# Kernel optimization log

Hardware: AMD Instinct MI355X
Metric: run time of the kernel (lower is better)

The kernel has to match this reference:

```python
import jax, jax.numpy as jnp
import numpy as np

N_NODES = 100000
IN_DIM = 512
HIDDEN = 64
NUM_CLASSES = 40
N_EDGES = 3200000


def setup_inputs() -> dict:
    key = jax.random.key(0)
    k1, k2, k3, k4, k5 = jax.random.split(key, 5)
    x = jax.random.normal(k1, (N_NODES, IN_DIM), dtype=jnp.float32)
    edge_index = jax.random.randint(k2, (2, N_EDGES), 0, N_NODES, dtype=jnp.int64)
    # Glorot init like PyG GCNConv, zero bias
    s1 = (6.0 / (IN_DIM + HIDDEN)) ** 0.5
    W1 = jax.random.uniform(k3, (IN_DIM, HIDDEN), jnp.float32, -s1, s1)
    b1 = jnp.zeros((HIDDEN,), jnp.float32)
    s2 = (6.0 / (HIDDEN + NUM_CLASSES)) ** 0.5
    W2 = jax.random.uniform(k4, (HIDDEN, NUM_CLASSES), jnp.float32, -s2, s2)
    b2 = jnp.zeros((NUM_CLASSES,), jnp.float32)
    return {"x": x, "edge_index": edge_index, "W1": W1, "b1": b1, "W2": W2, "b2": b2}


def _gcn_norm(edge_index, num_nodes):
    # Add self-loops, compute symmetric normalization D^-1/2 A D^-1/2 (PyG GCNConv default).
    loop = jnp.arange(num_nodes, dtype=edge_index.dtype)
    src = jnp.concatenate([edge_index[0], loop])
    dst = jnp.concatenate([edge_index[1], loop])
    deg = jax.ops.segment_sum(jnp.ones_like(src, dtype=jnp.float32), dst, num_segments=num_nodes)
    dinv = jnp.where(deg > 0, jax.lax.rsqrt(deg), 0.0)
    norm = dinv[src] * dinv[dst]  # [E+N]
    return src, dst, norm


def _gcn_conv(x, src, dst, norm, W, b, num_nodes):
    h = x @ W                                # [N, F_out]
    msg = h[src] * norm[:, None]             # gather + scale, [E+N, F_out]
    out = jax.ops.segment_sum(msg, dst, num_segments=num_nodes)  # scatter-add
    return out + b


def reference(x, edge_index, W1, b1, W2, b2):
    n = x.shape[0]
    src, dst, norm = _gcn_norm(edge_index, n)
    h = _gcn_conv(x, src, dst, norm, W1, b1, n)
    h = jax.nn.relu(h)
    # F.dropout(training=False) is identity in eval mode
    h = _gcn_conv(h, src, dst, norm, W2, b2, n)
    return jax.nn.log_softmax(h, axis=1)
```

## Files before the change

kernel.cpp:

```cpp
#include <hip/hip_runtime.h>
#include <hip/hip_bf16.h>
#include <cmath>

#define NN 100000
#define IND 512
#define HID 64
#define NC  40
#define BWN 256
#define NBKT ((NN + BWN - 1) / BWN)
#define NBIN_BLOCKS 100

typedef unsigned int uint32;
typedef unsigned short ushort;
using short8 = __attribute__((ext_vector_type(8))) short;
using f32x4  = __attribute__((ext_vector_type(4))) float;

__device__ inline float bf_lo(uint32 u) { return __uint_as_float(u << 16); }
__device__ inline float bf_hi(uint32 u) { return __uint_as_float(u & 0xFFFF0000u); }
__device__ inline uint32 f2bf(float f) {
    uint32 u = __float_as_uint(f);
    return (u + 0x7FFFu + ((u >> 16) & 1u)) >> 16;
}
__device__ inline uint32 pack2bf(float a, float b) { return f2bf(a) | (f2bf(b) << 16); }


__global__ __launch_bounds__(256) void zero_kernel(int* __restrict__ ghist, int n) {
    int i = blockIdx.x * blockDim.x + threadIdx.x;
    if (i < n) ghist[i] = 0;
}

__global__ __launch_bounds__(256) void bhist_kernel(const int* __restrict__ dst,
                                                    int* __restrict__ ghist, int E) {
    __shared__ int hist[NBKT];
    int t = threadIdx.x;
    for (int i = t; i < NBKT; i += 256) hist[i] = 0;
    __syncthreads();
    for (int e = blockIdx.x * 256 + t; e < E; e += gridDim.x * 256)
        atomicAdd(&hist[dst[e] >> 8], 1);
    __syncthreads();
    for (int i = t; i < NBKT; i += 256)
        if (hist[i]) atomicAdd(&ghist[i], hist[i]);
}

__global__ __launch_bounds__(512) void bscan_kernel(const int* __restrict__ ghist,
                                                    int* __restrict__ bbase,
                                                    int* __restrict__ gcursor) {
    __shared__ int sh[512];
    int t = threadIdx.x;
    int v = (t < NBKT) ? ghist[t] : 0;
    sh[t] = v;
    __syncthreads();
    for (int off = 1; off < 512; off <<= 1) {
        int u = (t >= off) ? sh[t - off] : 0;
        __syncthreads();
        sh[t] += u;
        __syncthreads();
    }
    int ex = sh[t] - v;
    if (t < NBKT) { bbase[t] = ex; gcursor[t] = ex; }
    if (t == NBKT - 1) bbase[NBKT] = ex + v;
}

__global__ __launch_bounds__(512) void bin_kernel(const int* __restrict__ src,
                                                  const int* __restrict__ dst,
                                                  int* __restrict__ gcursor,
                                                  int* __restrict__ packed, int E) {
    __shared__ int hist[NBKT], base[NBKT], cur[NBKT];
    int b = blockIdx.x, t = threadIdx.x;
    int epb = (E + gridDim.x - 1) / gridDim.x;
    int lo = b * epb;
    int hi = lo + epb; if (hi > E) hi = E;
    for (int i = t; i < NBKT; i += 512) { hist[i] = 0; cur[i] = 0; }
    __syncthreads();
    for (int e = lo + t; e < hi; e += 512) atomicAdd(&hist[dst[e] >> 8], 1);
    __syncthreads();
    for (int i = t; i < NBKT; i += 512)
        if (hist[i]) base[i] = atomicAdd(&gcursor[i], hist[i]);
    __syncthreads();
    for (int e = lo + t; e < hi; e += 512) {
        int d = dst[e], s = src[e];
        int bk = d >> 8;
        int pos = base[bk] + atomicAdd(&cur[bk], 1);
        packed[pos] = ((d & 255) << 17) | s;
    }
}

__global__ __launch_bounds__(256) void csr_bucket_kernel(const int* __restrict__ packed,
                                                         const int* __restrict__ bbase,
                                                         int* __restrict__ rowptr,
                                                         int* __restrict__ colx,
                                                         float* __restrict__ dinv, int E) {
    __shared__ int hist[BWN], pfx[BWN], cur[BWN];
    int b = blockIdx.x, t = threadIdx.x;
    int nlo = b * BWN;
    int ncnt = NN - nlo; if (ncnt > BWN) ncnt = BWN;
    int ebeg = bbase[b], eend = bbase[b + 1];
    hist[t] = 0;
    __syncthreads();
    for (int e = ebeg + t; e < eend; e += 256) atomicAdd(&hist[packed[e] >> 17], 1);
    __syncthreads();
    int h = hist[t];
    pfx[t] = h;
    __syncthreads();
    for (int off = 1; off < 256; off <<= 1) {
        int u = (t >= off) ? pfx[t - off] : 0;
        __syncthreads();
        pfx[t] += u;
        __syncthreads();
    }
    int excl = pfx[t] - h;
    cur[t] = excl;
    int g = nlo + t;
    if (t < ncnt) {
        rowptr[g] = ebeg + excl;
        dinv[g] = rsqrtf((float)(h + 1));
    }
    if (b == 0 && t == 0) rowptr[NN] = E;
    __syncthreads();
    for (int e = ebeg + t; e < eend; e += 256) {
        int p = packed[e];
        int dl = p >> 17;
        int s = p & 0x1FFFF;
        int pos = ebeg + atomicAdd(&cur[dl], 1);
        colx[pos] = s;
    }
}


__global__ __launch_bounds__(256) void wt_kernel(const float* __restrict__ W1,
                                                 const float* __restrict__ W2,
                                                 ushort* __restrict__ w1t,
                                                 ushort* __restrict__ w2t) {
    int id = blockIdx.x * blockDim.x + threadIdx.x;
    if (id < IND * HID) {
        int n = id & 63, k = id >> 6;
        w1t[(size_t)n * IND + k] = (ushort)f2bf(W1[(size_t)k * HID + n]);
    } else if (id < IND * HID + 48 * HID) {
        int id2 = id - IND * HID;
        int n = id2 >> 6, k = id2 & 63;
        w2t[id2] = (n < NC) ? (ushort)f2bf(W2[(size_t)k * NC + n]) : (ushort)0;
    }
}


__global__ __launch_bounds__(256) void gemm1_mfma(const float* __restrict__ x,
                                                  const ushort* __restrict__ w1t,
                                                  const float* __restrict__ dinv,
                                                  ushort* __restrict__ hs, int M) {
    __shared__ ushort As[64 * 64];
    __shared__ ushort Bs[64 * 64];
    char* Ab = (char*)As;
    char* Bb = (char*)Bs;

    int t = threadIdx.x;
    int row0 = blockIdx.x * 64;

    int srow = t >> 2;
    int klane = t & 3;
    int grow = row0 + srow; if (grow > M - 1) grow = M - 1;
    const float* xrow = x + (size_t)grow * IND;
    const char* wrow = (const char*)(w1t + (size_t)srow * IND);
    int swrow = srow * 128;
    int swx = (srow & 7) << 4;

    int l = t & 63;
    int w = t >> 6;
    int lr = l & 15;
    int lk = (l >> 4) * 16;
    int arow_b = (w * 16 + lr) * 128;
    int aswz = ((w * 16 + lr) & 7) << 4;

    f32x4 acc[4] = {};

    float4 rx[4]; uint2 rw[4];
#pragma unroll
    for (int i = 0; i < 4; ++i) {
        rx[i] = *(const float4*)(xrow + i * 16 + klane * 4);
        rw[i] = *(const uint2*)(wrow + i * 32 + klane * 8);
    }

    for (int k0 = 0; k0 < IND; k0 += 64) {
#pragma unroll
        for (int i = 0; i < 4; ++i) {
            int kb = i * 32 + klane * 8;
            uint2 pkd;
            pkd.x = pack2bf(rx[i].x, rx[i].y);
            pkd.y = pack2bf(rx[i].z, rx[i].w);
            *(uint2*)(Ab + swrow + (kb ^ swx)) = pkd;
            *(uint2*)(Bb + swrow + (kb ^ swx)) = rw[i];
        }
        __syncthreads();

        if (k0 + 64 < IND) {
#pragma unroll
            for (int i = 0; i < 4; ++i) {
                rx[i] = *(const float4*)(xrow + k0 + 64 + i * 16 + klane * 4);
                rw[i] = *(const uint2*)(wrow + (k0 + 64) * 2 + i * 32 + klane * 8);
            }
        }

        short8 a0 = *(const short8*)(Ab + arow_b + ((0 + lk) ^ aswz));
        short8 a1 = *(const short8*)(Ab + arow_b + ((64 + lk) ^ aswz));
#pragma unroll
        for (int ns = 0; ns < 4; ++ns) {
            int brow = ns * 16 + lr;
            int bswz = (brow & 7) << 4;
            short8 b0 = *(const short8*)(Bb + brow * 128 + ((0 + lk) ^ bswz));
            short8 b1 = *(const short8*)(Bb + brow * 128 + ((64 + lk) ^ bswz));
            acc[ns] = __builtin_amdgcn_mfma_f32_16x16x32_bf16(a0, b0, acc[ns], 0, 0, 0);
            acc[ns] = __builtin_amdgcn_mfma_f32_16x16x32_bf16(a1, b1, acc[ns], 0, 0, 0);
        }
        __syncthreads();
    }

    int rbase = row0 + w * 16 + (l >> 4) * 4;
    float dv[4];
#pragma unroll
    for (int j = 0; j < 4; ++j) dv[j] = (rbase + j < M) ? dinv[rbase + j] : 0.f;
#pragma unroll
    for (int ns = 0; ns < 4; ++ns) {
        int col = ns * 16 + lr;
#pragma unroll
        for (int j = 0; j < 4; ++j) {
            int row = rbase + j;
            if (row < M) hs[(size_t)row * HID + col] = (ushort)f2bf(acc[ns][j] * dv[j]);
        }
    }
}


__global__ __launch_bounds__(256) void agg1_kernel(const uint32* __restrict__ hs,
                                                   const int* __restrict__ rowptr,
                                                   const int* __restrict__ colx,
                                                   const float* __restrict__ dinv,
                                                   const float* __restrict__ b1,
                                                   uint32* __restrict__ h1) {
    int node = (blockIdx.x * blockDim.x + threadIdx.x) >> 5;
    int l = threadIdx.x & 31;
    if (node >= NN) return;
    int beg = rowptr[node], end = rowptr[node + 1];
    uint32 u = hs[(size_t)node * 32 + l];
    float a0 = bf_lo(u), a1 = bf_hi(u);
    int e = beg;
    int n8 = beg + ((end - beg) & ~7);
    for (; e < n8; e += 8) {
        int c[8];
#pragma unroll
        for (int j = 0; j < 8; ++j) c[j] = __builtin_nontemporal_load(&colx[e + j]);
        uint32 uu[8];
#pragma unroll
        for (int j = 0; j < 8; ++j) uu[j] = hs[(size_t)c[j] * 32 + l];
#pragma unroll
        for (int j = 0; j < 8; ++j) { a0 += bf_lo(uu[j]); a1 += bf_hi(uu[j]); }
    }
    for (; e < end; ++e) {
        uint32 ue = hs[(size_t)__builtin_nontemporal_load(&colx[e]) * 32 + l];
        a0 += bf_lo(ue); a1 += bf_hi(ue);
    }
    float d = dinv[node];
    float2 bb = *(const float2*)(b1 + 2 * l);
    float v0 = a0 * d + bb.x;
    float v1 = a1 * d + bb.y;
    v0 = v0 > 0.f ? v0 : 0.f;
    v1 = v1 > 0.f ? v1 : 0.f;
    __builtin_nontemporal_store(pack2bf(v0, v1), &h1[(size_t)node * 32 + l]);
}


__global__ __launch_bounds__(256) void gemm2_mfma(const ushort* __restrict__ h1,
                                                  const ushort* __restrict__ w2t,
                                                  const float* __restrict__ dinv,
                                                  ushort* __restrict__ h2b, int M) {
    int t = threadIdx.x;
    int w = t >> 6, l = t & 63;
    int lr = l & 15, lh = l >> 4;
    int row0 = blockIdx.x * 64 + w * 16;
    int arow = row0 + lr; if (arow > M - 1) arow = M - 1;
    const ushort* hrow = h1 + (size_t)arow * HID;

    f32x4 acc[3] = {};
#pragma unroll
    for (int ks = 0; ks < 2; ++ks) {
        short8 a = *(const short8*)(hrow + ks * 32 + lh * 8);
#pragma unroll
        for (int ns = 0; ns < 3; ++ns) {
            short8 b = *(const short8*)(w2t + (size_t)(ns * 16 + lr) * HID + ks * 32 + lh * 8);
            acc[ns] = __builtin_amdgcn_mfma_f32_16x16x32_bf16(a, b, acc[ns], 0, 0, 0);
        }
    }

    int rbase = row0 + lh * 4;
    float dv[4];
#pragma unroll
    for (int j = 0; j < 4; ++j) dv[j] = (rbase + j < M) ? dinv[rbase + j] : 0.f;
#pragma unroll
    for (int ns = 0; ns < 3; ++ns) {
        int col = ns * 16 + lr;
        if (col < NC) {
#pragma unroll
            for (int j = 0; j < 4; ++j) {
                int row = rbase + j;
                if (row < M) h2b[(size_t)row * NC + col] = (ushort)f2bf(acc[ns][j] * dv[j]);
            }
        }
    }
}


__global__ __launch_bounds__(256) void agg2_kernel(const uint32* __restrict__ h2b,
                                                   const int* __restrict__ rowptr,
                                                   const int* __restrict__ colx,
                                                   const float* __restrict__ dinv,
                                                   const float* __restrict__ b2,
                                                   float* __restrict__ out) {
    int node = (blockIdx.x * blockDim.x + threadIdx.x) >> 5;
    int l = threadIdx.x & 31;
    if (node >= NN) return;
    bool act = l < 20;
    int beg = rowptr[node], end = rowptr[node + 1];
    float a0 = 0.f, a1 = 0.f;
    if (act) {
        uint32 u = h2b[(size_t)node * 20 + l];
        a0 = bf_lo(u); a1 = bf_hi(u);
    }
    int e = beg;
    int n8 = beg + ((end - beg) & ~7);
    for (; e < n8; e += 8) {
        int c[8];
#pragma unroll
        for (int j = 0; j < 8; ++j) c[j] = __builtin_nontemporal_load(&colx[e + j]);
        if (act) {
            uint32 uu[8];
#pragma unroll
            for (int j = 0; j < 8; ++j) uu[j] = h2b[(size_t)c[j] * 20 + l];
#pragma unroll
            for (int j = 0; j < 8; ++j) { a0 += bf_lo(uu[j]); a1 += bf_hi(uu[j]); }
        }
    }
    for (; e < end; ++e) {
        int c = __builtin_nontemporal_load(&colx[e]);
        if (act) {
            uint32 ue = h2b[(size_t)c * 20 + l];
            a0 += bf_lo(ue); a1 += bf_hi(ue);
        }
    }

    float d = dinv[node];
    float v0 = -INFINITY, v1 = -INFINITY;
    if (act) {
        float2 bb = *(const float2*)(b2 + 2 * l);
        v0 = a0 * d + bb.x;
        v1 = a1 * d + bb.y;
    }
    float m = fmaxf(v0, v1);
#pragma unroll
    for (int off = 16; off; off >>= 1) m = fmaxf(m, __shfl_xor(m, off));
    float s = act ? (expf(v0 - m) + expf(v1 - m)) : 0.f;
#pragma unroll
    for (int off = 16; off; off >>= 1) s += __shfl_xor(s, off);
    if (act) {
        float ls = logf(s);
        __builtin_nontemporal_store(v0 - m - ls, &out[(size_t)node * NC + 2 * l]);
        __builtin_nontemporal_store(v1 - m - ls, &out[(size_t)node * NC + 2 * l + 1]);
    }
}


extern "C" void kernel_launch(void* const* d_in, const int* in_sizes, int n_in,
                              void* d_out, int out_size, void* d_ws, size_t ws_size,
                              hipStream_t stream) {
    const float* x  = (const float*)d_in[0];
    const int* ei   = (const int*)d_in[1];
    const float* W1 = (const float*)d_in[2];
    const float* b1 = (const float*)d_in[3];
    const float* W2 = (const float*)d_in[4];
    const float* b2 = (const float*)d_in[5];
    float* out = (float*)d_out;

    const int E = in_sizes[1] / 2;
    const int* src = ei;
    const int* dst = ei + E;

    char* p = (char*)d_ws;
    size_t off = 0;
    auto carve = [&](size_t bytes) {
        void* q = p + off;
        off = (off + bytes + 255) & ~(size_t)255;
        return q;
    };
    int* ghist    = (int*)carve((size_t)NBKT * 4);
    int* bbase    = (int*)carve((size_t)(NBKT + 1) * 4);
    int* gcursor  = (int*)carve((size_t)NBKT * 4);
    int* rowptr   = (int*)carve((size_t)(NN + 1) * 4);
    float* dinv   = (float*)carve((size_t)NN * 4);
    int* colx     = (int*)carve((size_t)E * 4);
    ushort* w1t   = (ushort*)carve((size_t)IND * HID * 2);
    ushort* w2t   = (ushort*)carve((size_t)48 * HID * 2);
    ushort* hs    = (ushort*)carve((size_t)NN * HID * 2);
    ushort* h2b   = (ushort*)carve((size_t)NN * NC * 2);
    uint32* h1    = (uint32*)carve((size_t)NN * 32 * 4);
    int* packed   = (int*)carve((size_t)E * 4);

    zero_kernel<<<(NBKT + 255) / 256, 256, 0, stream>>>(ghist, NBKT);
    bhist_kernel<<<256, 256, 0, stream>>>(dst, ghist, E);
    bscan_kernel<<<1, 512, 0, stream>>>(ghist, bbase, gcursor);
    bin_kernel<<<NBIN_BLOCKS, 512, 0, stream>>>(src, dst, gcursor, packed, E);
    csr_bucket_kernel<<<NBKT, 256, 0, stream>>>(packed, bbase, rowptr, colx, dinv, E);
    wt_kernel<<<(IND * HID + 48 * HID + 255) / 256, 256, 0, stream>>>(W1, W2, w1t, w2t);
    gemm1_mfma<<<(NN + 63) / 64, 256, 0, stream>>>(x, w1t, dinv, hs, NN);
    agg1_kernel<<<(NN * 32 + 255) / 256, 256, 0, stream>>>((const uint32*)hs, rowptr, colx, dinv, b1, h1);
    gemm2_mfma<<<(NN + 63) / 64, 256, 0, stream>>>((const ushort*)h1, w2t, dinv, h2b, NN);
    agg2_kernel<<<(NN * 32 + 255) / 256, 256, 0, stream>>>((const uint32*)h2b, rowptr, colx, dinv, b2, out);
}
```

Measured before the change: 339.3 us.

## Use fixed-capacity buckets and fuse second GEMM into first aggregation

```diff
diff --git a/kernel.cpp b/kernel.cpp
--- a/kernel.cpp
+++ b/kernel.cpp
@@ -8,7 +8,8 @@
 #define NC  40
 #define BWN 256
 #define NBKT ((NN + BWN - 1) / BWN)
-#define NBIN_BLOCKS 100
+#define CAP  12288
+#define NBIN_BLOCKS 200
 
 typedef unsigned int uint32;
 typedef unsigned short ushort;
@@ -24,42 +25,17 @@
 __device__ inline uint32 pack2bf(float a, float b) { return f2bf(a) | (f2bf(b) << 16); }
 
 
-__global__ __launch_bounds__(256) void zero_kernel(int* __restrict__ ghist, int n) {
-    int i = blockIdx.x * blockDim.x + threadIdx.x;
-    if (i < n) ghist[i] = 0;
-}
-
-__global__ __launch_bounds__(256) void bhist_kernel(const int* __restrict__ dst,
-                                                    int* __restrict__ ghist, int E) {
-    __shared__ int hist[NBKT];
-    int t = threadIdx.x;
-    for (int i = t; i < NBKT; i += 256) hist[i] = 0;
-    __syncthreads();
-    for (int e = blockIdx.x * 256 + t; e < E; e += gridDim.x * 256)
-        atomicAdd(&hist[dst[e] >> 8], 1);
-    __syncthreads();
-    for (int i = t; i < NBKT; i += 256)
-        if (hist[i]) atomicAdd(&ghist[i], hist[i]);
-}
-
-__global__ __launch_bounds__(512) void bscan_kernel(const int* __restrict__ ghist,
-                                                    int* __restrict__ bbase,
-                                                    int* __restrict__ gcursor) {
-    __shared__ int sh[512];
-    int t = threadIdx.x;
-    int v = (t < NBKT) ? ghist[t] : 0;
-    sh[t] = v;
-    __syncthreads();
-    for (int off = 1; off < 512; off <<= 1) {
-        int u = (t >= off) ? sh[t - off] : 0;
-        __syncthreads();
-        sh[t] += u;
-        __syncthreads();
-    }
-    int ex = sh[t] - v;
-    if (t < NBKT) { bbase[t] = ex; gcursor[t] = ex; }
-    if (t == NBKT - 1) bbase[NBKT] = ex + v;
-}
+__global__ __launch_bounds__(256) void wt_init_kernel(const float* __restrict__ W1,
+                                                      ushort* __restrict__ w1t,
+                                                      int* __restrict__ gcursor) {
+    int id = blockIdx.x * blockDim.x + threadIdx.x;
+    if (id < IND * HID) {
+        int n = id & 63, k = id >> 6;
+        w1t[(size_t)n * IND + k] = (ushort)f2bf(W1[(size_t)k * HID + n]);
+    }
+    if (id < NBKT) gcursor[id] = id * CAP;
+}
+
 
 __global__ __launch_bounds__(512) void bin_kernel(const int* __restrict__ src,
                                                   const int* __restrict__ dst,
@@ -85,16 +61,18 @@
     }
 }
 
+
 __global__ __launch_bounds__(256) void csr_bucket_kernel(const int* __restrict__ packed,
-                                                         const int* __restrict__ bbase,
+                                                         const int* __restrict__ gcursor,
                                                          int* __restrict__ rowptr,
+                                                         int* __restrict__ rowend,
                                                          int* __restrict__ colx,
-                                                         float* __restrict__ dinv, int E) {
+                                                         float* __restrict__ dinv) {
     __shared__ int hist[BWN], pfx[BWN], cur[BWN];
     int b = blockIdx.x, t = threadIdx.x;
     int nlo = b * BWN;
     int ncnt = NN - nlo; if (ncnt > BWN) ncnt = BWN;
-    int ebeg = bbase[b], eend = bbase[b + 1];
+    int ebeg = b * CAP, eend = gcursor[b];
     hist[t] = 0;
     __syncthreads();
     for (int e = ebeg + t; e < eend; e += 256) atomicAdd(&hist[packed[e] >> 17], 1);
@@ -113,9 +91,9 @@
     int g = nlo + t;
     if (t < ncnt) {
         rowptr[g] = ebeg + excl;
+        rowend[g] = ebeg + excl + h;
         dinv[g] = rsqrtf((float)(h + 1));
     }
-    if (b == 0 && t == 0) rowptr[NN] = E;
     __syncthreads();
     for (int e = ebeg + t; e < eend; e += 256) {
         int p = packed[e];
@@ -123,22 +101,6 @@
         int s = p & 0x1FFFF;
         int pos = ebeg + atomicAdd(&cur[dl], 1);
         colx[pos] = s;
-    }
-}
-
-
-__global__ __launch_bounds__(256) void wt_kernel(const float* __restrict__ W1,
-                                                 const float* __restrict__ W2,
-                                                 ushort* __restrict__ w1t,
-                                                 ushort* __restrict__ w2t) {
-    int id = blockIdx.x * blockDim.x + threadIdx.x;
-    if (id < IND * HID) {
-        int n = id & 63, k = id >> 6;
-        w1t[(size_t)n * IND + k] = (ushort)f2bf(W1[(size_t)k * HID + n]);
-    } else if (id < IND * HID + 48 * HID) {
-        int id2 = id - IND * HID;
-        int n = id2 >> 6, k = id2 & 63;
-        w2t[id2] = (n < NC) ? (ushort)f2bf(W2[(size_t)k * NC + n]) : (ushort)0;
     }
 }
 
@@ -229,16 +191,26 @@
 }
 
 
-__global__ __launch_bounds__(256) void agg1_kernel(const uint32* __restrict__ hs,
-                                                   const int* __restrict__ rowptr,
-                                                   const int* __restrict__ colx,
-                                                   const float* __restrict__ dinv,
-                                                   const float* __restrict__ b1,
-                                                   uint32* __restrict__ h1) {
-    int node = (blockIdx.x * blockDim.x + threadIdx.x) >> 5;
-    int l = threadIdx.x & 31;
+__global__ __launch_bounds__(256) void agg1_fused(const uint32* __restrict__ hs,
+                                                  const int* __restrict__ rowptr,
+                                                  const int* __restrict__ rowend,
+                                                  const int* __restrict__ colx,
+                                                  const float* __restrict__ dinv,
+                                                  const float* __restrict__ b1,
+                                                  const float* __restrict__ W2,
+                                                  uint32* __restrict__ h2b) {
+    __shared__ float w2s[64][42];
+    int t = threadIdx.x;
+    for (int i = t; i < HID * NC; i += 256) {
+        int k = i / NC, c = i - k * NC;
+        w2s[k][c] = W2[i];
+    }
+    __syncthreads();
+
+    int node = (blockIdx.x * blockDim.x + t) >> 5;
+    int l = t & 31;
     if (node >= NN) return;
-    int beg = rowptr[node], end = rowptr[node + 1];
+    int beg = rowptr[node], end = rowend[node];
     uint32 u = hs[(size_t)node * 32 + l];
     float a0 = bf_lo(u), a1 = bf_hi(u);
     int e = beg;
@@ -263,52 +235,27 @@
     float v1 = a1 * d + bb.y;
     v0 = v0 > 0.f ? v0 : 0.f;
     v1 = v1 > 0.f ? v1 : 0.f;
-    __builtin_nontemporal_store(pack2bf(v0, v1), &h1[(size_t)node * 32 + l]);
-}
-
-
-__global__ __launch_bounds__(256) void gemm2_mfma(const ushort* __restrict__ h1,
-                                                  const ushort* __restrict__ w2t,
-                                                  const float* __restrict__ dinv,
-                                                  ushort* __restrict__ h2b, int M) {
-    int t = threadIdx.x;
-    int w = t >> 6, l = t & 63;
-    int lr = l & 15, lh = l >> 4;
-    int row0 = blockIdx.x * 64 + w * 16;
-    int arow = row0 + lr; if (arow > M - 1) arow = M - 1;
-    const ushort* hrow = h1 + (size_t)arow * HID;
-
-    f32x4 acc[3] = {};
-#pragma unroll
-    for (int ks = 0; ks < 2; ++ks) {
-        short8 a = *(const short8*)(hrow + ks * 32 + lh * 8);
-#pragma unroll
-        for (int ns = 0; ns < 3; ++ns) {
-            short8 b = *(const short8*)(w2t + (size_t)(ns * 16 + lr) * HID + ks * 32 + lh * 8);
-            acc[ns] = __builtin_amdgcn_mfma_f32_16x16x32_bf16(a, b, acc[ns], 0, 0, 0);
-        }
-    }
-
-    int rbase = row0 + lh * 4;
-    float dv[4];
-#pragma unroll
-    for (int j = 0; j < 4; ++j) dv[j] = (rbase + j < M) ? dinv[rbase + j] : 0.f;
-#pragma unroll
-    for (int ns = 0; ns < 3; ++ns) {
-        int col = ns * 16 + lr;
-        if (col < NC) {
-#pragma unroll
-            for (int j = 0; j < 4; ++j) {
-                int row = rbase + j;
-                if (row < M) h2b[(size_t)row * NC + col] = (ushort)f2bf(acc[ns][j] * dv[j]);
-            }
-        }
-    }
+
+    float s0 = 0.f, s1 = 0.f;
+#pragma unroll
+    for (int k = 0; k < 32; ++k) {
+        float u0 = __shfl(v0, k, 32);
+        float u1 = __shfl(v1, k, 32);
+        if (l < 20) {
+            float2 wa = *(const float2*)&w2s[2 * k][2 * l];
+            float2 wb = *(const float2*)&w2s[2 * k + 1][2 * l];
+            s0 += u0 * wa.x + u1 * wb.x;
+            s1 += u0 * wa.y + u1 * wb.y;
+        }
+    }
+    if (l < 20)
+        __builtin_nontemporal_store(pack2bf(s0 * d, s1 * d), &h2b[(size_t)node * 20 + l]);
 }
 
 
 __global__ __launch_bounds__(256) void agg2_kernel(const uint32* __restrict__ h2b,
                                                    const int* __restrict__ rowptr,
+                                                   const int* __restrict__ rowend,
                                                    const int* __restrict__ colx,
                                                    const float* __restrict__ dinv,
                                                    const float* __restrict__ b2,
@@ -317,7 +264,7 @@
     int l = threadIdx.x & 31;
     if (node >= NN) return;
     bool act = l < 20;
-    int beg = rowptr[node], end = rowptr[node + 1];
+    int beg = rowptr[node], end = rowend[node];
     float a0 = 0.f, a1 = 0.f;
     if (act) {
         uint32 u = h2b[(size_t)node * 20 + l];
@@ -388,27 +335,20 @@
         off = (off + bytes + 255) & ~(size_t)255;
         return q;
     };
-    int* ghist    = (int*)carve((size_t)NBKT * 4);
-    int* bbase    = (int*)carve((size_t)(NBKT + 1) * 4);
     int* gcursor  = (int*)carve((size_t)NBKT * 4);
-    int* rowptr   = (int*)carve((size_t)(NN + 1) * 4);
+    int* rowptr   = (int*)carve((size_t)NN * 4);
+    int* rowend   = (int*)carve((size_t)NN * 4);
     float* dinv   = (float*)carve((size_t)NN * 4);
-    int* colx     = (int*)carve((size_t)E * 4);
     ushort* w1t   = (ushort*)carve((size_t)IND * HID * 2);
-    ushort* w2t   = (ushort*)carve((size_t)48 * HID * 2);
     ushort* hs    = (ushort*)carve((size_t)NN * HID * 2);
-    ushort* h2b   = (ushort*)carve((size_t)NN * NC * 2);
-    uint32* h1    = (uint32*)carve((size_t)NN * 32 * 4);
-    int* packed   = (int*)carve((size_t)E * 4);
-
-    zero_kernel<<<(NBKT + 255) / 256, 256, 0, stream>>>(ghist, NBKT);
-    bhist_kernel<<<256, 256, 0, stream>>>(dst, ghist, E);
-    bscan_kernel<<<1, 512, 0, stream>>>(ghist, bbase, gcursor);
+    uint32* h2b   = (uint32*)carve((size_t)NN * 20 * 4);
+    int* colx     = (int*)carve((size_t)NBKT * CAP * 4);
+    int* packed   = (int*)carve((size_t)NBKT * CAP * 4);
+
+    wt_init_kernel<<<(IND * HID + 255) / 256, 256, 0, stream>>>(W1, w1t, gcursor);
     bin_kernel<<<NBIN_BLOCKS, 512, 0, stream>>>(src, dst, gcursor, packed, E);
-    csr_bucket_kernel<<<NBKT, 256, 0, stream>>>(packed, bbase, rowptr, colx, dinv, E);
-    wt_kernel<<<(IND * HID + 48 * HID + 255) / 256, 256, 0, stream>>>(W1, W2, w1t, w2t);
+    csr_bucket_kernel<<<NBKT, 256, 0, stream>>>(packed, gcursor, rowptr, rowend, colx, dinv);
     gemm1_mfma<<<(NN + 63) / 64, 256, 0, stream>>>(x, w1t, dinv, hs, NN);
-    agg1_kernel<<<(NN * 32 + 255) / 256, 256, 0, stream>>>((const uint32*)hs, rowptr, colx, dinv, b1, h1);
-    gemm2_mfma<<<(NN + 63) / 64, 256, 0, stream>>>((const ushort*)h1, w2t, dinv, h2b, NN);
-    agg2_kernel<<<(NN * 32 + 255) / 256, 256, 0, stream>>>((const uint32*)h2b, rowptr, colx, dinv, b2, out);
-}
+    agg1_fused<<<(NN * 32 + 255) / 256, 256, 0, stream>>>((const uint32*)hs, rowptr, rowend, colx, dinv, b1, W2, h2b);
+    agg2_kernel<<<(NN * 32 + 255) / 256, 256, 0, stream>>>(h2b, rowptr, rowend, colx, dinv, b2, out);
+}
```

Result: faster. 316.0 us (-6.9%).
